# Performance work log

Hardware: AMD Instinct MI355X
Metric: run time of the kernel (lower is better)

The kernel has to match this reference:

```python
import jax, jax.numpy as jnp
import numpy as np
import math

B, L, D, H = 4, 2048, 768, 6
HD = D // H  # head_dim = 128

def setup_inputs() -> dict:
    key = jax.random.key(0)
    ks = jax.random.split(key, 9)
    s = 0.02
    return {
        "x": jax.random.normal(ks[0], (B, L, D), dtype=jnp.float32),
        "Wq": jax.random.normal(ks[1], (D, D), dtype=jnp.float32) * s,
        "bq": jnp.zeros((D,), dtype=jnp.float32),
        "Wk": jax.random.normal(ks[2], (D, D), dtype=jnp.float32) * s,
        "bk": jnp.zeros((D,), dtype=jnp.float32),
        "Wv": jax.random.normal(ks[3], (D, D), dtype=jnp.float32) * s,
        "bv": jnp.zeros((D,), dtype=jnp.float32),
        "Wo": jax.random.normal(ks[4], (D, D), dtype=jnp.float32) * s,
        "bo": jnp.zeros((D,), dtype=jnp.float32),
    }

def _split_heads(t):
    # [b, l, h*d] -> [b, h, l, d]
    b, l, _ = t.shape
    return t.reshape(b, l, H, HD).transpose(0, 2, 1, 3)

def reference(x, Wq, bq, Wk, bk, Wv, bv, Wo, bo):
    q = _split_heads(x @ Wq + bq)
    k = _split_heads(x @ Wk + bk)
    v = _split_heads(x @ Wv + bv)
    scores = jnp.einsum("bhqd,bhkd->bhqk", q, k) / math.sqrt(HD)
    # Original builds jnp.tril(ones, k=1) and fills mask==0 positions; it
    # mistakenly used +inf there, which yields NaN — we use -inf (intended
    # masking math) while keeping the same tril(k=1) pattern.
    l = x.shape[1]
    mask = jnp.tril(jnp.ones((l, l), dtype=bool), k=1)
    logits = jnp.where(mask, scores, -jnp.inf)
    attn = jax.nn.softmax(logits, axis=-1)
    out = jnp.einsum("bhqk,bhkd->bhqd", attn, v)
    out = out.transpose(0, 2, 1, 3).reshape(x.shape[0], l, D)
    # dropout in eval/deterministic mode: identity
    return out @ Wo + bo
```

## Files before the change

### kernel.cpp

```cpp
#include <hip/hip_runtime.h>
#include <math.h>

#define HEADS 6
#define SEQ   2048
#define DIM   768
#define HDIM  128
#define BATCH 4
#define MTOT  (BATCH*SEQ)
#define NKV   (SEQ/32)

typedef float  f32x4   __attribute__((ext_vector_type(4)));
typedef __bf16 bf16x8  __attribute__((ext_vector_type(8)));
typedef __bf16 bf16x4  __attribute__((ext_vector_type(4)));
typedef float  f32x4v  __attribute__((ext_vector_type(4)));

typedef __attribute__((address_space(3))) void lds_v;
typedef __attribute__((address_space(1))) void gbl_v;

__device__ __forceinline__ f32x4 mfma16(bf16x8 a, bf16x8 b, f32x4 c) {
    return __builtin_amdgcn_mfma_f32_16x16x32_bf16(a, b, c, 0, 0, 0);
}
__device__ __forceinline__ unsigned int bperm(int srclane, unsigned int v) {
    return (unsigned int)__builtin_amdgcn_ds_bpermute(srclane << 2, (int)v);
}
__device__ __forceinline__ unsigned int pack2(float lo, float hi) {
    union { __bf16 b; unsigned short u; } a, c;
    a.b = (__bf16)lo; c.b = (__bf16)hi;
    return ((unsigned int)c.u << 16) | (unsigned int)a.u;
}

__global__ __launch_bounds__(256) void prep_kernel(
    const float* __restrict__ x, __bf16* __restrict__ xb,
    const float* __restrict__ W0, const float* __restrict__ W1,
    const float* __restrict__ W2, const float* __restrict__ W3,
    __bf16* __restrict__ T0, __bf16* __restrict__ T1,
    __bf16* __restrict__ T2, __bf16* __restrict__ T3) {
    __shared__ float tile[32][33];
    if (blockIdx.x < 6144) {
        int i = (blockIdx.x * 256 + threadIdx.x) * 4;
        f32x4v v = *(const f32x4v*)(x + i);
        bf16x4 o;
        o[0] = (__bf16)v[0]; o[1] = (__bf16)v[1];
        o[2] = (__bf16)v[2]; o[3] = (__bf16)v[3];
        *(bf16x4*)(xb + i) = o;
        return;
    }
    const int bid = blockIdx.x - 6144;
    const int z = bid / 576, r = bid % 576;
    const int bx = r % 24, by = r / 24;
    const float* W; __bf16* T;
    if      (z == 0) { W = W0; T = T0; }
    else if (z == 1) { W = W1; T = T1; }
    else if (z == 2) { W = W2; T = T2; }
    else             { W = W3; T = T3; }
    int n0 = bx * 32, k0 = by * 32;
    int tx = threadIdx.x & 31, ty = threadIdx.x >> 5;
#pragma unroll
    for (int i = 0; i < 4; ++i)
        tile[ty + i*8][tx] = W[(size_t)(k0 + ty + i*8) * DIM + n0 + tx];
    __syncthreads();
#pragma unroll
    for (int i = 0; i < 4; ++i)
        T[(size_t)(n0 + ty + i*8) * DIM + k0 + tx] = (__bf16)tile[tx][ty + i*8];
}

#define GEMM_PIPE(A_PTR, B_PTR, NKSTEP)                                           \
    __shared__ __align__(16) __bf16 As[3][128 * 32];                              \
    __shared__ __align__(16) __bf16 Bs[3][128 * 32];                              \
    const int tid  = threadIdx.x;                                                 \
    const int wave = tid >> 6, lane = tid & 63;                                   \
    const int l16  = lane & 15, lh = lane >> 4;                                   \
    const int wr = wave >> 1, wc = wave & 1;                                      \
    f32x4 acc[4][4] = {};                                                         \
    auto stage = [&](int buf, int step) {                                         \
        const int k0 = step * 32;                                                 \
        _Pragma("unroll")                                                         \
        for (int ci = 0; ci < 4; ++ci) {                                          \
            int c = wave * 4 + ci;                                                \
            int t = c & 7;                                                        \
            int e = (t * 64 + lane) * 8;                                          \
            int r = e >> 5, kk = e & 31;                                          \
            const __bf16* gp = (c < 8) ? ((A_PTR) + (size_t)(m0 + r) * DIM + k0 + kk) \
                                       : ((B_PTR) + (size_t)(n0 + r) * DIM + k0 + kk); \
            __bf16* lp = (c < 8 ? As[buf] : Bs[buf]) + t * 512;                   \
            __builtin_amdgcn_global_load_lds((const gbl_v*)gp, (lds_v*)lp, 16, 0, 0); \
        }                                                                         \
    };                                                                            \
    stage(0, 0); stage(1, 1);                                                     \
    asm volatile("s_waitcnt vmcnt(4)" ::: "memory");                              \
    __builtin_amdgcn_s_barrier();                                                 \
    for (int t = 0; t < (NKSTEP); ++t) {                                          \
        const int cur = t % 3;                                                    \
        if (t + 2 < (NKSTEP)) stage((t + 2) % 3, t + 2);                          \
        bf16x8 af[4], bfr[4];                                                     \
        _Pragma("unroll")                                                         \
        for (int i = 0; i < 4; ++i)                                               \
            af[i] = *(const bf16x8*)&As[cur][(wr*64 + i*16 + l16) * 32 + lh*8];   \
        _Pragma("unroll")                                                         \
        for (int j = 0; j < 4; ++j)                                               \
            bfr[j] = *(const bf16x8*)&Bs[cur][(wc*64 + j*16 + l16) * 32 + lh*8];  \
        __builtin_amdgcn_s_setprio(1);                                            \
        _Pragma("unroll")                                                         \
        for (int i = 0; i < 4; ++i)                                               \
            _Pragma("unroll")                                                     \
            for (int j = 0; j < 4; ++j)                                           \
                acc[i][j] = mfma16(af[i], bfr[j], acc[i][j]);                     \
        __builtin_amdgcn_s_setprio(0);                                            \
        if (t + 2 < (NKSTEP))      asm volatile("s_waitcnt vmcnt(4)" ::: "memory"); \
        else if (t + 1 < (NKSTEP)) asm volatile("s_waitcnt vmcnt(0)" ::: "memory"); \
        __builtin_amdgcn_s_barrier();                                             \
    }

__global__ __launch_bounds__(256) void gemm_qkv(const __bf16* __restrict__ A,
                                                const __bf16* __restrict__ Wcat,
                                                const float* __restrict__ bq,
                                                const float* __restrict__ bk,
                                                const float* __restrict__ bv,
                                                __bf16* __restrict__ Qb,
                                                __bf16* __restrict__ Kb,
                                                __bf16* __restrict__ Vt) {
    constexpr int NWG = (MTOT/128) * (2304/128);
    const int swz = (blockIdx.x & 7) * (NWG >> 3) + (blockIdx.x >> 3);
    const int bn = swz % (2304 / 128), bm = swz / (2304 / 128);
    const int m0 = bm * 128, n0 = bn * 128;
    GEMM_PIPE(A, Wcat, 24)

    const int sel = n0 / DIM;
    const float* bias = sel == 0 ? bq : (sel == 1 ? bk : bv);
#pragma unroll
    for (int i = 0; i < 4; ++i) {
        int row = m0 + wr*64 + i*16 + lh*4;
#pragma unroll
        for (int j = 0; j < 4; ++j) {
            int col  = n0 + wc*64 + j*16 + l16;
            int lcol = col - sel * DIM;
            float bvv = bias[lcol];
            if (sel < 2) {
                __bf16* o = (sel == 0) ? Qb : Kb;
#pragma unroll
                for (int r = 0; r < 4; ++r)
                    o[(size_t)(row + r) * DIM + lcol] = (__bf16)(acc[i][j][r] + bvv);
            } else {
                int bb = row >> 11, ll = row & (SEQ - 1);
                int hh = lcol >> 7, dd = lcol & (HDIM - 1);
                bf16x4 pk;
#pragma unroll
                for (int r = 0; r < 4; ++r) pk[r] = (__bf16)(acc[i][j][r] + bvv);
                *(bf16x4*)&Vt[((size_t)((bb*HEADS + hh) * HDIM + dd)) * SEQ + ll] = pk;
            }
        }
    }
}

__global__ __launch_bounds__(256) void gemm_out(const __bf16* __restrict__ A,
                                                const __bf16* __restrict__ Bt,
                                                const float* __restrict__ bias,
                                                float* __restrict__ outp) {
    constexpr int NWG = (MTOT/128) * (DIM/128);
    const int swz = (blockIdx.x & 7) * (NWG >> 3) + (blockIdx.x >> 3);
    const int bn = swz % (DIM / 128), bm = swz / (DIM / 128);
    const int m0 = bm * 128, n0 = bn * 128;
    GEMM_PIPE(A, Bt, 24)

#pragma unroll
    for (int i = 0; i < 4; ++i) {
        int row = m0 + wr*64 + i*16 + lh*4;
#pragma unroll
        for (int j = 0; j < 4; ++j) {
            int col = n0 + wc*64 + j*16 + l16;
            float bv = bias[col];
#pragma unroll
            for (int r = 0; r < 4; ++r)
                outp[(size_t)(row + r) * DIM + col] = acc[i][j][r] + bv;
        }
    }
}

__global__ __launch_bounds__(256, 3) void attn_kernel(
    const __bf16* __restrict__ Q, const __bf16* __restrict__ K,
    const __bf16* __restrict__ Vt,
    __bf16* __restrict__ po, float* __restrict__ pm, float* __restrict__ pl,
    __bf16* __restrict__ Ob, int ks) {
    __shared__ __align__(16) __bf16 Ks[2][32 * 128];
    __shared__ __align__(16) __bf16 Vs[2][128 * 32];
    const int lane = threadIdx.x & 63, wv = threadIdx.x >> 6;
    const int l16 = lane & 15, lh = lane >> 4;
    const int id  = blockIdx.x;
    const int xcd = id & 7;
    const int idx = id >> 3;
    const int bh_l = idx % 3, rem = idx / 3;
    const int c = rem % ks, tl = rem / ks;
    const int tile = (tl & 1) ? (31 - (tl >> 1)) : (tl >> 1);
    const int bh = xcd + 8 * bh_l;
    const int b = bh / HEADS, h = bh - b * HEADS;
    const int qw0 = tile * 64 + wv * 16;
    const float qs = 0.12751674770951932f;

    bf16x8 qf[4];
    {
        const __bf16* qp = Q + (size_t)(b*SEQ + qw0 + l16) * DIM + h*HDIM + lh*8;
#pragma unroll
        for (int kk = 0; kk < 4; ++kk) {
            bf16x8 v = *(const bf16x8*)(qp + kk*32);
            bf16x8 sv;
#pragma unroll
            for (int e = 0; e < 8; ++e) sv[e] = (__bf16)((float)v[e] * qs);
            qf[kk] = sv;
        }
    }

    const __bf16* kgb = K  + (size_t)(b*SEQ) * DIM + h*HDIM;
    const __bf16* vgb = Vt + (size_t)bh * HDIM * SEQ;

    auto stage = [&](int buf, int kb) {
        const int kbase = kb * 32;
#pragma unroll
        for (int s = 0; s < 4; ++s) {
            const int j = wv * 4 + s;
            if (j < 8) {
                const int row = j * 4 + (lane >> 4);
                const int c16 = (lane & 15) ^ (row & 7);
                const __bf16* gp = kgb + (size_t)(kbase + row) * DIM + c16 * 8;
                __builtin_amdgcn_global_load_lds((const gbl_v*)gp,
                    (lds_v*)&Ks[buf][j * 512], 16, 0, 0);
            } else {
                const int jj = j - 8;
                const int row = jj * 16 + (lane >> 2);
                const int c16 = (lane & 3) ^ ((row >> 1) & 3);
                const __bf16* gp = vgb + (size_t)row * SEQ + kbase + c16 * 8;
                __builtin_amdgcn_global_load_lds((const gbl_v*)gp,
                    (lds_v*)&Vs[buf][jj * 512], 16, 0, 0);
            }
        }
    };

    f32x4 o[8] = {};
    float mx = -INFINITY, lsum = 0.f;
    const int nkb = min(2 * tile + 3, NKV);
    const int cnt = (nkb - c + ks - 1) / ks;

    stage(0, c);
    asm volatile("s_waitcnt vmcnt(0)" ::: "memory");
    __builtin_amdgcn_s_barrier();

    int cur = 0;
    for (int i = 0; i < cnt; ++i) {
        const int kb = c + i * ks;
        const int kbase = kb * 32;
        const bool more = (i + 1 < cnt);
        if (more) {
            stage(cur ^ 1, kb + ks);
            asm volatile("s_waitcnt vmcnt(4)" ::: "memory");
        } else {
            asm volatile("s_waitcnt vmcnt(0)" ::: "memory");
        }
        __builtin_amdgcn_s_barrier();

        if (kbase <= qw0 + 16) {
            bf16x8 kfA[4], kfB[4];
#pragma unroll
            for (int kk = 0; kk < 4; ++kk) {
                const int ca = (kk*4 + lh) ^ (l16 & 7);
                kfA[kk] = *(const bf16x8*)&Ks[cur][l16 * 128 + ca * 8];
                const int rb = 16 + l16;
                const int cb = (kk*4 + lh) ^ (rb & 7);
                kfB[kk] = *(const bf16x8*)&Ks[cur][rb * 128 + cb * 8];
            }
            f32x4 sA = {}, sB = {};
            __builtin_amdgcn_s_setprio(1);
#pragma unroll
            for (int kk = 0; kk < 4; ++kk) {
                sA = mfma16(kfA[kk], qf[kk], sA);
                sB = mfma16(kfB[kk], qf[kk], sB);
            }
            __builtin_amdgcn_s_setprio(0);
            const int q = qw0 + l16;
            float p[8];
#pragma unroll
            for (int r = 0; r < 4; ++r) { p[r] = sA[r]; p[r+4] = sB[r]; }
            if (kbase + 30 > qw0) {
#pragma unroll
                for (int r = 0; r < 4; ++r) {
                    const int key = kbase + lh*4 + r;
                    if (key      > q + 1) p[r]   = -INFINITY;
                    if (key + 16 > q + 1) p[r+4] = -INFINITY;
                }
            }
            float m0 = p[0];
#pragma unroll
            for (int t2 = 1; t2 < 8; ++t2) m0 = fmaxf(m0, p[t2]);
            m0 = fmaxf(m0, __shfl_xor(m0, 16));
            m0 = fmaxf(m0, __shfl_xor(m0, 32));
            const float mnew = fmaxf(mx, m0);
            const bool grow = m0 > mx;
            const float mref = (mnew == -INFINITY) ? 0.f : mnew;
#pragma unroll
            for (int t2 = 0; t2 < 8; ++t2) p[t2] = exp2f(p[t2] - mref);
            float rs = 0.f;
#pragma unroll
            for (int t2 = 0; t2 < 8; ++t2) rs += p[t2];
            rs += __shfl_xor(rs, 16);
            rs += __shfl_xor(rs, 32);
            if (__any(grow)) {
                const float resc = (mx < mnew) ? exp2f(mx - mnew) : 1.0f;
                lsum = lsum * resc + rs;
                mx = mnew;
#pragma unroll
                for (int d = 0; d < 8; ++d)
#pragma unroll
                    for (int r = 0; r < 4; ++r) o[d][r] *= resc;
            } else {
                lsum += rs;
            }
            unsigned int w0 = pack2(p[0], p[1]);
            unsigned int w1 = pack2(p[2], p[3]);
            unsigned int w2 = pack2(p[4], p[5]);
            unsigned int w3 = pack2(p[6], p[7]);
            const int s0l = l16 + ((lh & 1) << 5);
            unsigned int A0 = bperm(s0l,      w0), A1 = bperm(s0l,      w1);
            unsigned int A2 = bperm(s0l,      w2), A3 = bperm(s0l,      w3);
            unsigned int B0 = bperm(s0l + 16, w0), B1 = bperm(s0l + 16, w1);
            unsigned int B2 = bperm(s0l + 16, w2), B3 = bperm(s0l + 16, w3);
            const bool hi = (lh >= 2);
            union { unsigned int u[4]; bf16x8 v; } pu;
            pu.u[0] = hi ? A2 : A0;
            pu.u[1] = hi ? A3 : A1;
            pu.u[2] = hi ? B2 : B0;
            pu.u[3] = hi ? B3 : B1;
            const bf16x8 pf = pu.v;
            __builtin_amdgcn_s_setprio(1);
#pragma unroll
            for (int d = 0; d < 8; ++d) {
                const int row = d * 16 + l16;
                const int cv = lh ^ ((row >> 1) & 3);
                bf16x8 vf = *(const bf16x8*)&Vs[cur][row * 32 + cv * 8];
                o[d] = mfma16(vf, pf, o[d]);
            }
            __builtin_amdgcn_s_setprio(0);
        }
        __builtin_amdgcn_s_barrier();
        cur ^= 1;
    }

    if (ks == 1) {
        const float inv = 1.0f / lsum;
        __bf16* op = Ob + (size_t)(b*SEQ + qw0 + l16) * DIM + h*HDIM;
#pragma unroll
        for (int d = 0; d < 8; ++d) {
            bf16x4 pk;
#pragma unroll
            for (int r = 0; r < 4; ++r) pk[r] = (__bf16)(o[d][r] * inv);
            *(bf16x4*)(op + d*16 + lh*4) = pk;
        }
    } else {
        const int pid = (bh * 32 + tile) * ks + c;
        const int lq  = wv * 16 + l16;
        __bf16* pop = po + ((size_t)pid * 64 + lq) * HDIM;
#pragma unroll
        for (int d = 0; d < 8; ++d) {
            bf16x4 pk;
#pragma unroll
            for (int r = 0; r < 4; ++r) pk[r] = (__bf16)o[d][r];
            *(bf16x4*)(pop + d*16 + lh*4) = pk;
        }
        if (lh == 0) {
            pm[(size_t)pid * 64 + lq] = mx;
            pl[(size_t)pid * 64 + lq] = lsum;
        }
    }
}

__global__ __launch_bounds__(256) void merge_kernel(const __bf16* __restrict__ po,
    const float* __restrict__ pm, const float* __restrict__ pl,
    __bf16* __restrict__ Ob, int ks) {
    const int id = blockIdx.x;
    const int bh = id >> 5, tile = id & 31;
    const int b = bh / HEADS, h = bh - b * HEADS;
    const int lq = threadIdx.x >> 2;
    const int d0 = (threadIdx.x & 3) * 32;
    const int pb = id * ks;
    float M = -INFINITY;
    for (int cc = 0; cc < ks; ++cc) M = fmaxf(M, pm[(size_t)(pb + cc) * 64 + lq]);
    float L = 0.f, w[2] = {0.f, 0.f};
    for (int cc = 0; cc < ks; ++cc) {
        w[cc] = exp2f(pm[(size_t)(pb + cc) * 64 + lq] - M);
        L += w[cc] * pl[(size_t)(pb + cc) * 64 + lq];
    }
    const float invL = 1.0f / L;
    __bf16* op = Ob + (size_t)(b*SEQ + tile*64 + lq) * DIM + h*HDIM;
#pragma unroll
    for (int d = 0; d < 32; d += 8) {
        float acc[8] = {};
        for (int cc = 0; cc < ks; ++cc) {
            bf16x8 v = *(const bf16x8*)&po[((size_t)(pb + cc) * 64 + lq) * HDIM + d0 + d];
            const float wc = w[cc];
#pragma unroll
            for (int e = 0; e < 8; ++e) acc[e] += wc * (float)v[e];
        }
        bf16x8 ov;
#pragma unroll
        for (int e = 0; e < 8; ++e) ov[e] = (__bf16)(acc[e] * invL);
        *(bf16x8*)(op + d0 + d) = ov;
    }
}

extern "C" void kernel_launch(void* const* d_in, const int* in_sizes, int n_in,
                              void* d_out, int out_size, void* d_ws, size_t ws_size,
                              hipStream_t stream) {
    const float* x  = (const float*)d_in[0];
    const float* Wq = (const float*)d_in[1];
    const float* bq = (const float*)d_in[2];
    const float* Wk = (const float*)d_in[3];
    const float* bk = (const float*)d_in[4];
    const float* Wv = (const float*)d_in[5];
    const float* bv = (const float*)d_in[6];
    const float* Wo = (const float*)d_in[7];
    const float* bo = (const float*)d_in[8];

    char* p = (char*)d_ws;
    const size_t SZ_X = (size_t)MTOT * DIM * 2;
    const size_t SZ_W = (size_t)DIM * DIM * 2;
    __bf16* xb   = (__bf16*)p; p += SZ_X;
    __bf16* Wcat = (__bf16*)p; p += 3 * SZ_W;
    __bf16* Wto  = (__bf16*)p; p += SZ_W;
    __bf16* Qb   = (__bf16*)p; p += SZ_X;
    __bf16* Kb   = (__bf16*)p; p += SZ_X;
    __bf16* Vt   = (__bf16*)p; p += SZ_X;
    __bf16* Ob   = (__bf16*)p; p += SZ_X;

    const size_t base = (size_t)(p - (char*)d_ws);
    const size_t SZ_PO = (size_t)24 * 32 * 2 * 64 * HDIM * 2;
    const size_t SZ_PM = (size_t)24 * 32 * 2 * 64 * 4;
    const int ks = (ws_size >= base + SZ_PO + 2 * SZ_PM) ? 2 : 1;
    __bf16* po = (__bf16*)p;            p += SZ_PO;
    float*  pmv = (float*)p;            p += SZ_PM;
    float*  plv = (float*)p;

    prep_kernel<<<6144 + 2304, 256, 0, stream>>>(
        x, xb, Wq, Wk, Wv, Wo,
        Wcat, Wcat + (size_t)DIM*DIM, Wcat + (size_t)2*DIM*DIM, Wto);

    gemm_qkv<<<(MTOT/128) * (2304/128), 256, 0, stream>>>(xb, Wcat, bq, bk, bv, Qb, Kb, Vt);

    attn_kernel<<<768 * ks, 256, 0, stream>>>(Qb, Kb, Vt, po, pmv, plv, Ob, ks);
    if (ks == 2)
        merge_kernel<<<24 * 32, 256, 0, stream>>>(po, pmv, plv, Ob, ks);

    gemm_out<<<(MTOT/128) * (DIM/128), 256, 0, stream>>>(Ob, Wto, bo, (float*)d_out);
}
```

Measured before the change: 172.5 us.

## Split causal attention into fixed-size KV chunks with variable per-tile split count

Replaces the uniform 2-way strided KV split with contiguous chunks of 16 KV blocks, so longer causal tiles get up to 4 chunks and short tiles get one. Each block does a bounded amount of work, and the heaviest chunks are scheduled first, which should balance load across CUs. Multi-chunk tiles are merged by a merge kernel that now handles up to 4 partials. The output buffer now reuses the xb workspace, and the partial-buffer allocation no longer checks ws_size, which risks overflow if the workspace is too small.

```diff
diff --git a/kernel.cpp b/kernel.cpp
--- a/kernel.cpp
+++ b/kernel.cpp
@@ -8,6 +8,7 @@
 #define BATCH 4
 #define MTOT  (BATCH*SEQ)
 #define NKV   (SEQ/32)
+#define NCHUNK_TOT 83
 
 typedef float  f32x4   __attribute__((ext_vector_type(4)));
 typedef __bf16 bf16x8  __attribute__((ext_vector_type(8)));
@@ -180,7 +181,7 @@
     const __bf16* __restrict__ Q, const __bf16* __restrict__ K,
     const __bf16* __restrict__ Vt,
     __bf16* __restrict__ po, float* __restrict__ pm, float* __restrict__ pl,
-    __bf16* __restrict__ Ob, int ks) {
+    __bf16* __restrict__ Ob) {
     __shared__ __align__(16) __bf16 Ks[2][32 * 128];
     __shared__ __align__(16) __bf16 Vs[2][128 * 32];
     const int lane = threadIdx.x & 63, wv = threadIdx.x >> 6;
@@ -188,12 +189,21 @@
     const int id  = blockIdx.x;
     const int xcd = id & 7;
     const int idx = id >> 3;
-    const int bh_l = idx % 3, rem = idx / 3;
-    const int c = rem % ks, tl = rem / ks;
-    const int tile = (tl & 1) ? (31 - (tl >> 1)) : (tl >> 1);
+    const int bh_l = idx % 3;
+    const int ci = (NCHUNK_TOT - 1) - idx / 3;
+    int tile, chunk;
+    if      (ci < 7)  { tile = ci;                chunk = 0;          }
+    else if (ci < 23) { tile = 7  + (ci-7)/2;     chunk = (ci-7)&1;   }
+    else if (ci < 47) { tile = 15 + (ci-23)/3;    chunk = (ci-23)%3;  }
+    else              { tile = 23 + (ci-47)/4;    chunk = (ci-47)&3;  }
+    const int cstart = ci - chunk;
     const int bh = xcd + 8 * bh_l;
     const int b = bh / HEADS, h = bh - b * HEADS;
     const int qw0 = tile * 64 + wv * 16;
+    const int nkb = min(2 * tile + 3, NKV);
+    const int nc  = (nkb + 15) >> 4;
+    const int lo  = chunk * 16;
+    const int cnt = min(lo + 16, nkb) - lo;
     const float qs = 0.12751674770951932f;
 
     bf16x8 qf[4];
@@ -236,20 +246,18 @@
 
     f32x4 o[8] = {};
     float mx = -INFINITY, lsum = 0.f;
-    const int nkb = min(2 * tile + 3, NKV);
-    const int cnt = (nkb - c + ks - 1) / ks;
-
-    stage(0, c);
+
+    stage(0, lo);
     asm volatile("s_waitcnt vmcnt(0)" ::: "memory");
     __builtin_amdgcn_s_barrier();
 
     int cur = 0;
     for (int i = 0; i < cnt; ++i) {
-        const int kb = c + i * ks;
+        const int kb = lo + i;
         const int kbase = kb * 32;
         const bool more = (i + 1 < cnt);
         if (more) {
-            stage(cur ^ 1, kb + ks);
+            stage(cur ^ 1, kb + 1);
             asm volatile("s_waitcnt vmcnt(4)" ::: "memory");
         } else {
             asm volatile("s_waitcnt vmcnt(0)" ::: "memory");
@@ -342,7 +350,7 @@
         cur ^= 1;
     }
 
-    if (ks == 1) {
+    if (nc == 1) {
         const float inv = 1.0f / lsum;
         __bf16* op = Ob + (size_t)(b*SEQ + qw0 + l16) * DIM + h*HDIM;
 #pragma unroll
@@ -353,7 +361,7 @@
             *(bf16x4*)(op + d*16 + lh*4) = pk;
         }
     } else {
-        const int pid = (bh * 32 + tile) * ks + c;
+        const int pid = bh * NCHUNK_TOT + cstart + chunk;
         const int lq  = wv * 16 + l16;
         __bf16* pop = po + ((size_t)pid * 64 + lq) * HDIM;
 #pragma unroll
@@ -372,27 +380,32 @@
 
 __global__ __launch_bounds__(256) void merge_kernel(const __bf16* __restrict__ po,
     const float* __restrict__ pm, const float* __restrict__ pl,
-    __bf16* __restrict__ Ob, int ks) {
+    __bf16* __restrict__ Ob) {
     const int id = blockIdx.x;
-    const int bh = id >> 5, tile = id & 31;
+    const int bh = id / 25;
+    const int tile = 7 + id % 25;
+    int cstart, nc;
+    if      (tile < 15) { cstart = 7  + (tile-7)*2;   nc = 2; }
+    else if (tile < 23) { cstart = 23 + (tile-15)*3;  nc = 3; }
+    else                { cstart = 47 + (tile-23)*4;  nc = 4; }
     const int b = bh / HEADS, h = bh - b * HEADS;
     const int lq = threadIdx.x >> 2;
     const int d0 = (threadIdx.x & 3) * 32;
-    const int pb = id * ks;
+    const size_t pb = (size_t)bh * NCHUNK_TOT + cstart;
     float M = -INFINITY;
-    for (int cc = 0; cc < ks; ++cc) M = fmaxf(M, pm[(size_t)(pb + cc) * 64 + lq]);
-    float L = 0.f, w[2] = {0.f, 0.f};
-    for (int cc = 0; cc < ks; ++cc) {
-        w[cc] = exp2f(pm[(size_t)(pb + cc) * 64 + lq] - M);
-        L += w[cc] * pl[(size_t)(pb + cc) * 64 + lq];
+    for (int cc = 0; cc < nc; ++cc) M = fmaxf(M, pm[(pb + cc) * 64 + lq]);
+    float L = 0.f, w[4] = {0.f, 0.f, 0.f, 0.f};
+    for (int cc = 0; cc < nc; ++cc) {
+        w[cc] = exp2f(pm[(pb + cc) * 64 + lq] - M);
+        L += w[cc] * pl[(pb + cc) * 64 + lq];
     }
     const float invL = 1.0f / L;
     __bf16* op = Ob + (size_t)(b*SEQ + tile*64 + lq) * DIM + h*HDIM;
 #pragma unroll
     for (int d = 0; d < 32; d += 8) {
         float acc[8] = {};
-        for (int cc = 0; cc < ks; ++cc) {
-            bf16x8 v = *(const bf16x8*)&po[((size_t)(pb + cc) * 64 + lq) * HDIM + d0 + d];
+        for (int cc = 0; cc < nc; ++cc) {
+            bf16x8 v = *(const bf16x8*)&po[((pb + cc) * 64 + lq) * HDIM + d0 + d];
             const float wc = w[cc];
 #pragma unroll
             for (int e = 0; e < 8; ++e) acc[e] += wc * (float)v[e];
@@ -426,13 +439,11 @@
     __bf16* Qb   = (__bf16*)p; p += SZ_X;
     __bf16* Kb   = (__bf16*)p; p += SZ_X;
     __bf16* Vt   = (__bf16*)p; p += SZ_X;
-    __bf16* Ob   = (__bf16*)p; p += SZ_X;
-
-    const size_t base = (size_t)(p - (char*)d_ws);
-    const size_t SZ_PO = (size_t)24 * 32 * 2 * 64 * HDIM * 2;
-    const size_t SZ_PM = (size_t)24 * 32 * 2 * 64 * 4;
-    const int ks = (ws_size >= base + SZ_PO + 2 * SZ_PM) ? 2 : 1;
-    __bf16* po = (__bf16*)p;            p += SZ_PO;
+    __bf16* Ob   = xb;
+
+    const size_t SZ_PO = (size_t)24 * NCHUNK_TOT * 64 * HDIM * 2;
+    const size_t SZ_PM = (size_t)24 * NCHUNK_TOT * 64 * 4;
+    __bf16* po  = (__bf16*)p;           p += SZ_PO;
     float*  pmv = (float*)p;            p += SZ_PM;
     float*  plv = (float*)p;
 
@@ -442,9 +453,8 @@
 
     gemm_qkv<<<(MTOT/128) * (2304/128), 256, 0, stream>>>(xb, Wcat, bq, bk, bv, Qb, Kb, Vt);
 
-    attn_kernel<<<768 * ks, 256, 0, stream>>>(Qb, Kb, Vt, po, pmv, plv, Ob, ks);
-    if (ks == 2)
-        merge_kernel<<<24 * 32, 256, 0, stream>>>(po, pmv, plv, Ob, ks);
+    attn_kernel<<<8 * 3 * NCHUNK_TOT, 256, 0, stream>>>(Qb, Kb, Vt, po, pmv, plv, Ob);
+    merge_kernel<<<24 * 25, 256, 0, stream>>>(po, pmv, plv, Ob);
 
     gemm_out<<<(MTOT/128) * (DIM/128), 256, 0, stream>>>(Ob, Wto, bo, (float*)d_out);
 }
```

Result: faster. 168.4 us (-2.4%).
